# Kernel optimization log

Measured on AMD Instinct MI355X. Metric: run time of the kernel, lower is better.

The kernel has to match this reference:

```python
import jax, jax.numpy as jnp
import numpy as np

B, N, D, DH = 2, 256, 256, 256


def setup_inputs() -> dict:
    key = jax.random.key(0)
    ks = jax.random.split(key, 8)
    s = 1.0 / np.sqrt(D)
    return {
        "x": jax.random.normal(ks[0], (B, N, D), dtype=jnp.float32),
        "e": jax.random.normal(ks[1], (B, N, N, D), dtype=jnp.float32),
        "Wq": jax.random.normal(ks[2], (D, DH), dtype=jnp.float32) * s,
        "bq": jnp.zeros((DH,), dtype=jnp.float32),
        "Wk": jax.random.normal(ks[3], (D, DH), dtype=jnp.float32) * s,
        "bk": jnp.zeros((DH,), dtype=jnp.float32),
        "Wv": jax.random.normal(ks[4], (D, DH), dtype=jnp.float32) * s,
        "bv": jnp.zeros((DH,), dtype=jnp.float32),
    }


def reference(x, e, Wq, bq, Wk, bk, Wv, bv):
    # Q_edge: [B, N, N, DH]; indexed Q[b, j, i, :]
    Q = jnp.einsum("bjid,dh->bjih", e, Wq) + bq
    K = x @ Wk + bk  # [B, N, DH]
    V = x @ Wv + bv  # [B, N, DH]
    scale = 1.0 / jnp.sqrt(jnp.asarray(Q.shape[-1], Q.dtype))
    # K_i[b,j,i] = K[b,i];  K_j[b,j,i] = K[b,j]  (torch expand semantics)
    att_i = jnp.exp(jnp.einsum("bjih,bih->bji", Q, K) * scale)
    att_j = jnp.exp(jnp.einsum("bjih,bjh->bji", Q, K) * scale)
    att_sum = att_i + att_j
    ai = att_i / att_sum  # dropout with p=0.0 is identity
    aj = att_j / att_sum
    # e_out[b,j,i] = ai*V[b,i] + aj*V[b,j]
    e_out = ai[..., None] * V[:, None, :, :] + aj[..., None] * V[:, :, None, :]
    return (x, e_out)
```

## Files before the change

### kernel.cpp

```cpp
#include <hip/hip_runtime.h>
#include <hip/hip_bf16.h>

typedef float nt4 __attribute__((ext_vector_type(4)));

constexpr int Bc  = 2;
constexpr int Nc  = 256;
constexpr int Dc  = 256;
constexpr int DHc = 256;

__device__ __forceinline__ float dpp_sum16(float v) {
    float t;
    t = __int_as_float(__builtin_amdgcn_mov_dpp(__float_as_int(v), 0xB1, 0xF, 0xF, true)); v += t;
    t = __int_as_float(__builtin_amdgcn_mov_dpp(__float_as_int(v), 0x4E, 0xF, 0xF, true)); v += t;
    t = __int_as_float(__builtin_amdgcn_mov_dpp(__float_as_int(v), 0x141, 0xF, 0xF, true)); v += t;
    t = __int_as_float(__builtin_amdgcn_mov_dpp(__float_as_int(v), 0x140, 0xF, 0xF, true)); v += t;
    return v;
}

__global__ __launch_bounds__(256)
void prep_gvc(const float* __restrict__ x,
              const float* __restrict__ Wq, const float* __restrict__ bq,
              const float* __restrict__ Wk, const float* __restrict__ bk,
              const float* __restrict__ Wv, const float* __restrict__ bv,
              float* __restrict__ G, float* __restrict__ V, float* __restrict__ cc,
              float* __restrict__ xout) {
    constexpr int RPB = 4;
    constexpr float scale = 0.0625f;
    __shared__ float xs[RPB][Dc];
    __shared__ float ks[RPB][DHc];
    const int r0 = blockIdx.x * RPB;
    const int dd = threadIdx.x;

    #pragma unroll
    for (int rr = 0; rr < RPB; ++rr) {
        float xv = x[(size_t)(r0 + rr) * Dc + dd];
        xs[rr][dd] = xv;
        xout[(size_t)(r0 + rr) * Dc + dd] = xv;
    }
    __syncthreads();

    float ka[RPB], va[RPB];
    {
        float bkv = bk[dd], bvv = bv[dd];
        #pragma unroll
        for (int rr = 0; rr < RPB; ++rr) { ka[rr] = bkv; va[rr] = bvv; }
    }
    #pragma unroll 4
    for (int d0 = 0; d0 < Dc; ++d0) {
        float wk = Wk[(size_t)d0 * DHc + dd];
        float wv = Wv[(size_t)d0 * DHc + dd];
        #pragma unroll
        for (int rr = 0; rr < RPB; ++rr) {
            ka[rr] += xs[rr][d0] * wk;
            va[rr] += xs[rr][d0] * wv;
        }
    }
    #pragma unroll
    for (int rr = 0; rr < RPB; ++rr) {
        ks[rr][dd] = ka[rr];
        V[(size_t)(r0 + rr) * DHc + dd] = va[rr];
    }
    __syncthreads();

    float ga[RPB] = {};
    #pragma unroll 8
    for (int h = 0; h < DHc; ++h) {
        float wq = Wq[(size_t)dd * DHc + h];
        #pragma unroll
        for (int rr = 0; rr < RPB; ++rr) ga[rr] += ks[rr][h] * wq;
    }
    #pragma unroll
    for (int rr = 0; rr < RPB; ++rr)
        G[(size_t)(r0 + rr) * Dc + dd] = ga[rr] * scale;

    {
        int rr = dd >> 6, l = dd & 63;
        float p = 0.f;
        #pragma unroll
        for (int k = 0; k < 4; ++k) p += ks[rr][l + 64 * k] * bq[l + 64 * k];
        #pragma unroll
        for (int m = 1; m < 64; m <<= 1) p += __shfl_xor(p, m, 64);
        if (l == 0) cc[r0 + rr] = p * scale;
    }
}

__global__ __launch_bounds__(256)
void score_pass(const float* __restrict__ e,
                const float* __restrict__ G,
                const float* __restrict__ cc,
                float* __restrict__ ai_out) {
    const int W = blockIdx.x * 4 + (threadIdx.x >> 6);
    const int l = threadIdx.x & 63;
    const int b   = W >> 12;
    const int rem = W & 4095;
    const int j   = rem >> 4;
    const int seg = rem & 15;
    const int g   = l >> 4;
    const int c4  = l & 15;
    const int r0  = seg * 16;

    const size_t nb = (size_t)b * Nc;
    const float4* G4 = reinterpret_cast<const float4*>(G);

    const float4 gj0 = G4[(nb + j) * 64 + c4];
    const float4 gj1 = G4[(nb + j) * 64 + c4 + 16];
    const float4 gj2 = G4[(nb + j) * 64 + c4 + 32];
    const float4 gj3 = G4[(nb + j) * 64 + c4 + 48];
    const float  cj  = cc[nb + j];

    const float4* e4  = reinterpret_cast<const float4*>(e) +
                        (((size_t)b * Nc + j) * Nc + r0) * 64;
    const float4* Gi  = G4 + (nb + r0) * 64;
    const float*  ccp = cc + nb + r0;
    float* aout = ai_out + ((size_t)b * Nc + j) * Nc + r0;

    #pragma unroll
    for (int t = 0; t < 4; ++t) {
        const int r = t * 4 + g;
        const float ci = ccp[r];
        float4 ev0 = e4[(size_t)r * 64 + c4];
        float4 ev1 = e4[(size_t)r * 64 + c4 + 16];
        float4 ev2 = e4[(size_t)r * 64 + c4 + 32];
        float4 ev3 = e4[(size_t)r * 64 + c4 + 48];
        float4 gi0 = Gi[(size_t)r * 64 + c4];
        float4 gi1 = Gi[(size_t)r * 64 + c4 + 16];
        float4 gi2 = Gi[(size_t)r * 64 + c4 + 32];
        float4 gi3 = Gi[(size_t)r * 64 + c4 + 48];

        float si, sj;
        si  = ev0.x * gi0.x + ev0.y * gi0.y + ev0.z * gi0.z + ev0.w * gi0.w;
        si += ev1.x * gi1.x + ev1.y * gi1.y + ev1.z * gi1.z + ev1.w * gi1.w;
        si += ev2.x * gi2.x + ev2.y * gi2.y + ev2.z * gi2.z + ev2.w * gi2.w;
        si += ev3.x * gi3.x + ev3.y * gi3.y + ev3.z * gi3.z + ev3.w * gi3.w;
        sj  = ev0.x * gj0.x + ev0.y * gj0.y + ev0.z * gj0.z + ev0.w * gj0.w;
        sj += ev1.x * gj1.x + ev1.y * gj1.y + ev1.z * gj1.z + ev1.w * gj1.w;
        sj += ev2.x * gj2.x + ev2.y * gj2.y + ev2.z * gj2.z + ev2.w * gj2.w;
        sj += ev3.x * gj3.x + ev3.y * gj3.y + ev3.z * gj3.z + ev3.w * gj3.w;

        si = dpp_sum16(si) + ci;
        sj = dpp_sum16(sj) + cj;
        const float ai = 1.f / (1.f + __expf(sj - si));
        if (c4 == 0) aout[r] = ai;
    }
}

__global__ __launch_bounds__(256)
void combine_pass(const float* __restrict__ ai_in,
                  const float* __restrict__ V,
                  float* __restrict__ eout) {
    const int W = blockIdx.x * 4 + (threadIdx.x >> 6);
    const int l = threadIdx.x & 63;
    const int b   = W >> 12;
    const int rem = W & 4095;
    const int j   = rem >> 4;
    const int seg = rem & 15;
    const int r0  = seg * 16;

    const size_t nb = (size_t)b * Nc;
    const float4* V4 = reinterpret_cast<const float4*>(V);
    const float4 vj = V4[(nb + j) * 64 + l];
    const float  av = ai_in[((size_t)b * Nc + j) * Nc + r0 + (l & 15)];

    const float4* Vi = V4 + (nb + r0) * 64 + l;
    float4* o4 = reinterpret_cast<float4*>(eout) +
                 (((size_t)b * Nc + j) * Nc + r0) * 64 + l;

    #pragma unroll
    for (int t = 0; t < 16; ++t) {
        const float ai = __int_as_float(
            __builtin_amdgcn_readlane(__float_as_int(av), t));
        const float aj = 1.f - ai;
        const float4 vi = Vi[(size_t)t * 64];
        nt4 o;
        o.x = ai * vi.x + aj * vj.x;
        o.y = ai * vi.y + aj * vj.y;
        o.z = ai * vi.z + aj * vj.z;
        o.w = ai * vi.w + aj * vj.w;
        __builtin_nontemporal_store(o, reinterpret_cast<nt4*>(&o4[(size_t)t * 64]));
    }
}

extern "C" void kernel_launch(void* const* d_in, const int* in_sizes, int n_in,
                              void* d_out, int out_size, void* d_ws, size_t ws_size,
                              hipStream_t stream) {
    const float* x  = (const float*)d_in[0];
    const float* e  = (const float*)d_in[1];
    const float* Wq = (const float*)d_in[2];
    const float* bq = (const float*)d_in[3];
    const float* Wk = (const float*)d_in[4];
    const float* bk = (const float*)d_in[5];
    const float* Wv = (const float*)d_in[6];
    const float* bv = (const float*)d_in[7];
    float* out = (float*)d_out;

    float* G  = (float*)d_ws;
    float* V  = G + (size_t)Bc * Nc * Dc;
    float* cc = V + (size_t)Bc * Nc * DHc;
    float* ai = cc + (size_t)Bc * Nc;

    float* eo = out + (size_t)Bc * Nc * Dc;

    prep_gvc<<<Bc * Nc / 4, 256, 0, stream>>>(x, Wq, bq, Wk, bk, Wv, bv,
                                              G, V, cc, out);
    score_pass<<<Bc * Nc * 16 / 4, 256, 0, stream>>>(e, G, cc, ai);
    combine_pass<<<Bc * Nc * 16 / 4, 256, 0, stream>>>(ai, V, eo);
}
```

Measured before the change: 291.0 us.

## Fuse score and combine passes into a single edge kernel

Merges the score kernel and the combine kernel into one edge kernel that computes attention weights and immediately writes the blended V output. This removes the intermediate ai buffer round-trip and one kernel launch. Each 16-lane group now handles two rows per iteration, which adds memory-level parallelism. The cost is higher register pressure, since G, V and e fragments are all live at once, and that may reduce occupancy.

Result: no change. 292.9 us (+0.6%).

```diff
diff --git a/kernel.cpp b/kernel.cpp
--- a/kernel.cpp
+++ b/kernel.cpp
@@ -85,69 +85,11 @@
 }
 
 __global__ __launch_bounds__(256)
-void score_pass(const float* __restrict__ e,
+void edge_fused(const float* __restrict__ e,
                 const float* __restrict__ G,
+                const float* __restrict__ V,
                 const float* __restrict__ cc,
-                float* __restrict__ ai_out) {
-    const int W = blockIdx.x * 4 + (threadIdx.x >> 6);
-    const int l = threadIdx.x & 63;
-    const int b   = W >> 12;
-    const int rem = W & 4095;
-    const int j   = rem >> 4;
-    const int seg = rem & 15;
-    const int g   = l >> 4;
-    const int c4  = l & 15;
-    const int r0  = seg * 16;
-
-    const size_t nb = (size_t)b * Nc;
-    const float4* G4 = reinterpret_cast<const float4*>(G);
-
-    const float4 gj0 = G4[(nb + j) * 64 + c4];
-    const float4 gj1 = G4[(nb + j) * 64 + c4 + 16];
-    const float4 gj2 = G4[(nb + j) * 64 + c4 + 32];
-    const float4 gj3 = G4[(nb + j) * 64 + c4 + 48];
-    const float  cj  = cc[nb + j];
-
-    const float4* e4  = reinterpret_cast<const float4*>(e) +
-                        (((size_t)b * Nc + j) * Nc + r0) * 64;
-    const float4* Gi  = G4 + (nb + r0) * 64;
-    const float*  ccp = cc + nb + r0;
-    float* aout = ai_out + ((size_t)b * Nc + j) * Nc + r0;
-
-    #pragma unroll
-    for (int t = 0; t < 4; ++t) {
-        const int r = t * 4 + g;
-        const float ci = ccp[r];
-        float4 ev0 = e4[(size_t)r * 64 + c4];
-        float4 ev1 = e4[(size_t)r * 64 + c4 + 16];
-        float4 ev2 = e4[(size_t)r * 64 + c4 + 32];
-        float4 ev3 = e4[(size_t)r * 64 + c4 + 48];
-        float4 gi0 = Gi[(size_t)r * 64 + c4];
-        float4 gi1 = Gi[(size_t)r * 64 + c4 + 16];
-        float4 gi2 = Gi[(size_t)r * 64 + c4 + 32];
-        float4 gi3 = Gi[(size_t)r * 64 + c4 + 48];
-
-        float si, sj;
-        si  = ev0.x * gi0.x + ev0.y * gi0.y + ev0.z * gi0.z + ev0.w * gi0.w;
-        si += ev1.x * gi1.x + ev1.y * gi1.y + ev1.z * gi1.z + ev1.w * gi1.w;
-        si += ev2.x * gi2.x + ev2.y * gi2.y + ev2.z * gi2.z + ev2.w * gi2.w;
-        si += ev3.x * gi3.x + ev3.y * gi3.y + ev3.z * gi3.z + ev3.w * gi3.w;
-        sj  = ev0.x * gj0.x + ev0.y * gj0.y + ev0.z * gj0.z + ev0.w * gj0.w;
-        sj += ev1.x * gj1.x + ev1.y * gj1.y + ev1.z * gj1.z + ev1.w * gj1.w;
-        sj += ev2.x * gj2.x + ev2.y * gj2.y + ev2.z * gj2.z + ev2.w * gj2.w;
-        sj += ev3.x * gj3.x + ev3.y * gj3.y + ev3.z * gj3.z + ev3.w * gj3.w;
-
-        si = dpp_sum16(si) + ci;
-        sj = dpp_sum16(sj) + cj;
-        const float ai = 1.f / (1.f + __expf(sj - si));
-        if (c4 == 0) aout[r] = ai;
-    }
-}
-
-__global__ __launch_bounds__(256)
-void combine_pass(const float* __restrict__ ai_in,
-                  const float* __restrict__ V,
-                  float* __restrict__ eout) {
+                float* __restrict__ eout) {
     const int W = blockIdx.x * 4 + (threadIdx.x >> 6);
     const int l = threadIdx.x & 63;
     const int b   = W >> 12;
@@ -155,28 +97,90 @@
     const int j   = rem >> 4;
     const int seg = rem & 15;
     const int r0  = seg * 16;
+    const int g   = l >> 4;
+    const int c4  = l & 15;
 
     const size_t nb = (size_t)b * Nc;
+    const float4* G4 = reinterpret_cast<const float4*>(G);
     const float4* V4 = reinterpret_cast<const float4*>(V);
-    const float4 vj = V4[(nb + j) * 64 + l];
-    const float  av = ai_in[((size_t)b * Nc + j) * Nc + r0 + (l & 15)];
-
-    const float4* Vi = V4 + (nb + r0) * 64 + l;
+
+    float4 gj[4], vj[4];
+    #pragma unroll
+    for (int k = 0; k < 4; ++k) {
+        gj[k] = G4[(nb + j) * 64 + c4 + 16 * k];
+        vj[k] = V4[(nb + j) * 64 + c4 + 16 * k];
+    }
+    const float cj = cc[nb + j];
+
+    const float4* e4  = reinterpret_cast<const float4*>(e) +
+                        (((size_t)b * Nc + j) * Nc + r0) * 64;
     float4* o4 = reinterpret_cast<float4*>(eout) +
-                 (((size_t)b * Nc + j) * Nc + r0) * 64 + l;
-
-    #pragma unroll
-    for (int t = 0; t < 16; ++t) {
-        const float ai = __int_as_float(
-            __builtin_amdgcn_readlane(__float_as_int(av), t));
-        const float aj = 1.f - ai;
-        const float4 vi = Vi[(size_t)t * 64];
-        nt4 o;
-        o.x = ai * vi.x + aj * vj.x;
-        o.y = ai * vi.y + aj * vj.y;
-        o.z = ai * vi.z + aj * vj.z;
-        o.w = ai * vi.w + aj * vj.w;
-        __builtin_nontemporal_store(o, reinterpret_cast<nt4*>(&o4[(size_t)t * 64]));
+                 (((size_t)b * Nc + j) * Nc + r0) * 64;
+    const float4* Gi  = G4 + (nb + r0) * 64;
+    const float4* Vi  = V4 + (nb + r0) * 64;
+    const float*  ccp = cc + nb + r0;
+
+    #pragma unroll
+    for (int u = 0; u < 2; ++u) {
+        const int rA = u * 8 + g * 2;
+        const int rB = rA + 1;
+
+        float4 evA[4], evB[4], giA[4], giB[4];
+        #pragma unroll
+        for (int k = 0; k < 4; ++k) evA[k] = e4[(size_t)rA * 64 + c4 + 16 * k];
+        #pragma unroll
+        for (int k = 0; k < 4; ++k) evB[k] = e4[(size_t)rB * 64 + c4 + 16 * k];
+        #pragma unroll
+        for (int k = 0; k < 4; ++k) giA[k] = Gi[(size_t)rA * 64 + c4 + 16 * k];
+        #pragma unroll
+        for (int k = 0; k < 4; ++k) giB[k] = Gi[(size_t)rB * 64 + c4 + 16 * k];
+        const float ciA = ccp[rA];
+        const float ciB = ccp[rB];
+
+        float siA = 0.f, sjA = 0.f, siB = 0.f, sjB = 0.f;
+        #pragma unroll
+        for (int k = 0; k < 4; ++k) {
+            siA += evA[k].x * giA[k].x + evA[k].y * giA[k].y +
+                   evA[k].z * giA[k].z + evA[k].w * giA[k].w;
+            siB += evB[k].x * giB[k].x + evB[k].y * giB[k].y +
+                   evB[k].z * giB[k].z + evB[k].w * giB[k].w;
+            sjA += evA[k].x * gj[k].x + evA[k].y * gj[k].y +
+                   evA[k].z * gj[k].z + evA[k].w * gj[k].w;
+            sjB += evB[k].x * gj[k].x + evB[k].y * gj[k].y +
+                   evB[k].z * gj[k].z + evB[k].w * gj[k].w;
+        }
+
+        siA = dpp_sum16(siA); sjA = dpp_sum16(sjA);
+        siB = dpp_sum16(siB); sjB = dpp_sum16(sjB);
+        siA += ciA; sjA += cj;
+        siB += ciB; sjB += cj;
+        const float aiA = 1.f / (1.f + __expf(sjA - siA));
+        const float aiB = 1.f / (1.f + __expf(sjB - siB));
+        const float ajA = 1.f - aiA;
+        const float ajB = 1.f - aiB;
+
+        float4 viA[4], viB[4];
+        #pragma unroll
+        for (int k = 0; k < 4; ++k) viA[k] = Vi[(size_t)rA * 64 + c4 + 16 * k];
+        #pragma unroll
+        for (int k = 0; k < 4; ++k) viB[k] = Vi[(size_t)rB * 64 + c4 + 16 * k];
+
+        #pragma unroll
+        for (int k = 0; k < 4; ++k) {
+            nt4 oA, oB;
+            oA.x = aiA * viA[k].x + ajA * vj[k].x;
+            oA.y = aiA * viA[k].y + ajA * vj[k].y;
+            oA.z = aiA * viA[k].z + ajA * vj[k].z;
+            oA.w = aiA * viA[k].w + ajA * vj[k].w;
+            oB.x = aiB * viB[k].x + ajB * vj[k].x;
+            oB.y = aiB * viB[k].y + ajB * vj[k].y;
+            oB.z = aiB * viB[k].z + ajB * vj[k].z;
+            oB.w = aiB * viB[k].w + ajB * vj[k].w;
+            __builtin_nontemporal_store(
+                oA, reinterpret_cast<nt4*>(&o4[(size_t)rA * 64 + c4 + 16 * k]));
+            __builtin_nontemporal_store(
+                oB, reinterpret_cast<nt4*>(&o4[(size_t)rB * 64 + c4 + 16 * k]));
+        }
     }
 }
 
@@ -196,12 +200,10 @@
     float* G  = (float*)d_ws;
     float* V  = G + (size_t)Bc * Nc * Dc;
     float* cc = V + (size_t)Bc * Nc * DHc;
-    float* ai = cc + (size_t)Bc * Nc;
 
     float* eo = out + (size_t)Bc * Nc * Dc;
 
     prep_gvc<<<Bc * Nc / 4, 256, 0, stream>>>(x, Wq, bq, Wk, bk, Wv, bv,
                                               G, V, cc, out);
-    score_pass<<<Bc * Nc * 16 / 4, 256, 0, stream>>>(e, G, cc, ai);
-    combine_pass<<<Bc * Nc * 16 / 4, 256, 0, stream>>>(ai, V, eo);
-}
+    edge_fused<<<Bc * Nc * 16 / 4, 256, 0, stream>>>(e, G, V, cc, eo);
+}
```
